# Kernel tuning notes

Hardware: AMD Instinct MI355X
Metric: run time of the kernel (lower is better)

Reference implementation:

```python
import jax, jax.numpy as jnp
import numpy as np

H = 8192  # hidden_size == input_size
NNZ = 1_000_000
B = 128
T = 64


def _spmm(rows, cols, values, x, out_dim):
    # y[r, :] += v * x[c, :] for each nnz (r, c, v); matches coalesced COO spmm
    gathered = values[:, None] * x[cols]          # [nnz, B]
    return jax.ops.segment_sum(gathered, rows, num_segments=out_dim)  # [out_dim, B]


def setup_inputs() -> dict:
    key = jax.random.key(0)
    ks = jax.random.split(key, 5)
    x = jax.random.normal(ks[0], (B, T, H), dtype=jnp.float32)
    ih_indices = jax.random.randint(ks[1], (2, NNZ), 0, H, dtype=jnp.int32)
    hh_indices = jax.random.randint(ks[2], (2, NNZ), 0, H, dtype=jnp.int32)
    # scale so tanh pre-activations stay in a reasonable range (~122 nnz/row)
    ih_values = jax.random.normal(ks[3], (NNZ,), dtype=jnp.float32) * 0.05
    hh_values = jax.random.normal(ks[4], (NNZ,), dtype=jnp.float32) * 0.05
    bias_ih = jnp.zeros((H, 1), dtype=jnp.float32)
    bias_hh = jnp.zeros((H, 1), dtype=jnp.float32)
    return {
        "x": x,
        "ih_indices": ih_indices,
        "ih_values": ih_values,
        "hh_indices": hh_indices,
        "hh_values": hh_values,
        "bias_ih": bias_ih,
        "bias_hh": bias_hh,
    }


def reference(x, ih_indices, ih_values, hh_indices, hh_values, bias_ih, bias_hh):
    # x: (batch, seq, features) -> (T, F, B) as in torch permute(1, 2, 0)
    xs = jnp.transpose(x, (1, 2, 0))  # [T, H, B]
    ih_r, ih_c = ih_indices[0], ih_indices[1]
    hh_r, hh_c = hh_indices[0], hh_indices[1]

    def step(h, x_t):
        pre = (_spmm(ih_r, ih_c, ih_values, x_t, H) + bias_ih
               + _spmm(hh_r, hh_c, hh_values, h, H) + bias_hh)
        h_new = jnp.tanh(pre)
        return h_new, h_new

    h0 = jnp.zeros((H, x.shape[0]), dtype=x.dtype)
    _, out = jax.lax.scan(step, h0, xs)  # out: [T, H, B]
    return jnp.transpose(out, (2, 0, 1))  # [B, T, H] (batch_first)
```

## Files before the change

kernel.cpp:

```cpp
#include <hip/hip_runtime.h>
#include <cstdint>
#include <cstddef>
#include <cstring>

#define H 8192
#define NNZ 1000000
#define B 128
#define T 64

typedef unsigned int u32;
typedef float f32x4 __attribute__((ext_vector_type(4)));

__device__ inline float bf_lo(u32 w) { return __uint_as_float(w << 16); }
__device__ inline float bf_hi(u32 w) { return __uint_as_float(w & 0xffff0000u); }
__device__ inline unsigned short f2bf(float f) {
    u32 v = __float_as_uint(f);
    v += 0x7fffu + ((v >> 16) & 1u);
    return (unsigned short)(v >> 16);
}
__device__ inline u32 pack_bf16(float a, float b) {
    return (u32)f2bf(a) | ((u32)f2bf(b) << 16);
}
__device__ inline float fast_tanh(float x) {
    float e = __expf(2.0f * x);
    return 1.0f - 2.0f / (e + 1.0f);
}

__global__ void hist_kernel(const int* __restrict__ rows, int nnz, int* __restrict__ count) {
    int j = blockIdx.x * blockDim.x + threadIdx.x;
    if (j < nnz) atomicAdd(&count[rows[j]], 1);
}

__global__ void scan_kernel(const int* __restrict__ cnt0, int* __restrict__ rp0, int* __restrict__ cur0,
                            const int* __restrict__ cnt1, int* __restrict__ rp1, int* __restrict__ cur1) {
    const int* cnt = (blockIdx.x == 0) ? cnt0 : cnt1;
    int* rp  = (blockIdx.x == 0) ? rp0 : rp1;
    int* cur = (blockIdx.x == 0) ? cur0 : cur1;
    __shared__ int buf[1024];
    __shared__ int carry;
    int tid = threadIdx.x;
    if (tid == 0) carry = 0;
    __syncthreads();
    for (int base = 0; base < H; base += 1024) {
        int v = cnt[base + tid];
        buf[tid] = v;
        __syncthreads();
        for (int off = 1; off < 1024; off <<= 1) {
            int t = (tid >= off) ? buf[tid - off] : 0;
            __syncthreads();
            buf[tid] += t;
            __syncthreads();
        }
        int incl = buf[tid];
        int excl = incl - v;
        int c = carry;
        rp[base + tid]  = c + excl;
        cur[base + tid] = c + excl;
        __syncthreads();
        if (tid == 1023) carry = c + incl;
        __syncthreads();
    }
    if (tid == 0) rp[H] = carry;
}

__global__ void scatter_kernel(const int* __restrict__ rows, const int* __restrict__ cols,
                               const float* __restrict__ vals, int nnz,
                               int* __restrict__ cursor, int2* __restrict__ opair) {
    int j = blockIdx.x * blockDim.x + threadIdx.x;
    if (j < nnz) {
        int r = rows[j];
        int p = atomicAdd(&cursor[r], 1);
        opair[p] = make_int2(cols[j], __float_as_int(vals[j]));
    }
}

__global__ void transpose_kernel(const float* __restrict__ src, float* __restrict__ dst,
                                 int R, int C) {
    __shared__ float tile[32][33];
    int c0 = blockIdx.x * 32, r0 = blockIdx.y * 32;
    int x = threadIdx.x, y = threadIdx.y;
    #pragma unroll
    for (int i = y; i < 32; i += 8) {
        tile[i][x] = src[(size_t)(r0 + i) * C + (c0 + x)];
    }
    __syncthreads();
    #pragma unroll
    for (int i = y; i < 32; i += 8) {
        dst[(size_t)(c0 + i) * R + (r0 + x)] = tile[x][i];
    }
}

__global__ void transpose_bf16_kernel(const float* __restrict__ src, u32* __restrict__ dst) {
    __shared__ float tile[32][33];
    int c0 = blockIdx.x * 32;
    int r0 = blockIdx.y * 32;
    int x = threadIdx.x, y = threadIdx.y;
    #pragma unroll
    for (int i = y; i < 32; i += 8) {
        tile[i][x] = src[(size_t)(r0 + i) * (T * H) + (c0 + x)];
    }
    __syncthreads();
    int tid = y * 32 + x;
    #pragma unroll
    for (int idx = tid; idx < 32 * 16; idx += 256) {
        int row = idx >> 4, w = idx & 15;
        u32 word = pack_bf16(tile[2 * w][row], tile[2 * w + 1][row]);
        dst[(size_t)(c0 + row) * 64 + (r0 >> 1) + w] = word;
    }
}

__global__ void __launch_bounds__(64) ih_pre_kernel(
    const int* __restrict__ rp, const int2* __restrict__ pair,
    const u32* __restrict__ xTb, float* __restrict__ pre,
    const float* __restrict__ bias_ih, const float* __restrict__ bias_hh) {
    int bid = blockIdx.x;
    int xcd = bid & 7;
    int i0  = bid >> 3;
    int t   = (xcd << 3) + (i0 >> 13);
    int r   = i0 & (H - 1);
    int lane = threadIdx.x;
    bool hi = lane >= 32;
    int i = lane & 31;
    const uint2* __restrict__ xt = (const uint2*)(xTb + (size_t)t * H * 64);
    f32x4 acc = {0.f, 0.f, 0.f, 0.f};
    int s = rp[r], e = rp[r + 1];
    int j = s;
    for (; j + 16 <= e; j += 16) {
        int2 q[16];
        #pragma unroll
        for (int u = 0; u < 16; ++u) q[u] = pair[j + u];
        uint2 g[8];
        #pragma unroll
        for (int u = 0; u < 8; ++u) {
            int c = hi ? q[2 * u + 1].x : q[2 * u].x;
            g[u] = xt[(size_t)c * 32 + i];
        }
        #pragma unroll
        for (int u = 0; u < 8; ++u) {
            float v = __int_as_float(hi ? q[2 * u + 1].y : q[2 * u].y);
            acc.x = fmaf(v, bf_lo(g[u].x), acc.x);
            acc.y = fmaf(v, bf_hi(g[u].x), acc.y);
            acc.z = fmaf(v, bf_lo(g[u].y), acc.z);
            acc.w = fmaf(v, bf_hi(g[u].y), acc.w);
        }
    }
    for (; j + 2 <= e; j += 2) {
        int2 q0 = pair[j], q1 = pair[j + 1];
        int c = hi ? q1.x : q0.x;
        uint2 g = xt[(size_t)c * 32 + i];
        float v = __int_as_float(hi ? q1.y : q0.y);
        acc.x = fmaf(v, bf_lo(g.x), acc.x);
        acc.y = fmaf(v, bf_hi(g.x), acc.y);
        acc.z = fmaf(v, bf_lo(g.y), acc.z);
        acc.w = fmaf(v, bf_hi(g.y), acc.w);
    }
    if (j < e) {
        int2 q0 = pair[j];
        uint2 g = xt[(size_t)q0.x * 32 + i];
        float v = hi ? 0.0f : __int_as_float(q0.y);
        acc.x = fmaf(v, bf_lo(g.x), acc.x);
        acc.y = fmaf(v, bf_hi(g.x), acc.y);
        acc.z = fmaf(v, bf_lo(g.y), acc.z);
        acc.w = fmaf(v, bf_hi(g.y), acc.w);
    }
    f32x4 tot;
    tot.x = acc.x + __shfl_xor(acc.x, 32, 64);
    tot.y = acc.y + __shfl_xor(acc.y, 32, 64);
    tot.z = acc.z + __shfl_xor(acc.z, 32, 64);
    tot.w = acc.w + __shfl_xor(acc.w, 32, 64);
    if (lane < 32) {
        float bias = bias_ih[r] + bias_hh[r];
        tot.x += bias; tot.y += bias; tot.z += bias; tot.w += bias;
        __builtin_nontemporal_store(tot, (f32x4*)(pre + ((size_t)t * H + r) * B) + i);
    }
}

__global__ void __launch_bounds__(64) step_kernel(
    const int* __restrict__ rp, const int2* __restrict__ pair,
    const u32* __restrict__ hprev, u32* __restrict__ hnew, float* __restrict__ pre_t) {
    int r = blockIdx.x;
    int lane = threadIdx.x;
    bool hi = lane >= 32;
    int i = lane & 31;
    const uint2* __restrict__ hp = (const uint2*)hprev;
    f32x4 acc = {0.f, 0.f, 0.f, 0.f};
    int s = rp[r], e = rp[r + 1];
    int j = s;
    for (; j + 16 <= e; j += 16) {
        int2 q[16];
        #pragma unroll
        for (int u = 0; u < 16; ++u) q[u] = pair[j + u];
        uint2 g[8];
        #pragma unroll
        for (int u = 0; u < 8; ++u) {
            int c = hi ? q[2 * u + 1].x : q[2 * u].x;
            g[u] = hp[(size_t)c * 32 + i];
        }
        #pragma unroll
        for (int u = 0; u < 8; ++u) {
            float v = __int_as_float(hi ? q[2 * u + 1].y : q[2 * u].y);
            acc.x = fmaf(v, bf_lo(g[u].x), acc.x);
            acc.y = fmaf(v, bf_hi(g[u].x), acc.y);
            acc.z = fmaf(v, bf_lo(g[u].y), acc.z);
            acc.w = fmaf(v, bf_hi(g[u].y), acc.w);
        }
    }
    for (; j + 2 <= e; j += 2) {
        int2 q0 = pair[j], q1 = pair[j + 1];
        int c = hi ? q1.x : q0.x;
        uint2 g = hp[(size_t)c * 32 + i];
        float v = __int_as_float(hi ? q1.y : q0.y);
        acc.x = fmaf(v, bf_lo(g.x), acc.x);
        acc.y = fmaf(v, bf_hi(g.x), acc.y);
        acc.z = fmaf(v, bf_lo(g.y), acc.z);
        acc.w = fmaf(v, bf_hi(g.y), acc.w);
    }
    if (j < e) {
        int2 q0 = pair[j];
        uint2 g = hp[(size_t)q0.x * 32 + i];
        float v = hi ? 0.0f : __int_as_float(q0.y);
        acc.x = fmaf(v, bf_lo(g.x), acc.x);
        acc.y = fmaf(v, bf_hi(g.x), acc.y);
        acc.z = fmaf(v, bf_lo(g.y), acc.z);
        acc.w = fmaf(v, bf_hi(g.y), acc.w);
    }
    f32x4 tot;
    tot.x = acc.x + __shfl_xor(acc.x, 32, 64);
    tot.y = acc.y + __shfl_xor(acc.y, 32, 64);
    tot.z = acc.z + __shfl_xor(acc.z, 32, 64);
    tot.w = acc.w + __shfl_xor(acc.w, 32, 64);
    if (lane < 32) {
        f32x4 p = __builtin_nontemporal_load((const f32x4*)(pre_t + (size_t)r * B) + i);
        float h0 = fast_tanh(tot.x + p.x);
        float h1 = fast_tanh(tot.y + p.y);
        float h2 = fast_tanh(tot.z + p.z);
        float h3 = fast_tanh(tot.w + p.w);
        f32x4 o = {h0, h1, h2, h3};
        __builtin_nontemporal_store(o, (f32x4*)(pre_t + (size_t)r * B) + i);
        uint2 hw;
        hw.x = pack_bf16(h0, h1);
        hw.y = pack_bf16(h2, h3);
        ((uint2*)hnew)[(size_t)r * 32 + i] = hw;
    }
}

extern "C" void kernel_launch(void* const* d_in, const int* in_sizes, int n_in,
                              void* d_out, int out_size, void* d_ws, size_t ws_size,
                              hipStream_t stream) {
    const float* x        = (const float*)d_in[0];
    const int*   ih_idx   = (const int*)d_in[1];
    const float* ih_val   = (const float*)d_in[2];
    const int*   hh_idx   = (const int*)d_in[3];
    const float* hh_val   = (const float*)d_in[4];
    const float* bias_ih  = (const float*)d_in[5];
    const float* bias_hh  = (const float*)d_in[6];
    const int* ih_rows = ih_idx;
    const int* ih_cols = ih_idx + NNZ;
    const int* hh_rows = hh_idx;
    const int* hh_cols = hh_idx + NNZ;

    char* ws = (char*)d_ws;
    size_t off = 0;
    auto alloc = [&](size_t bytes) -> void* {
        void* p = ws + off;
        off += (bytes + 255) & ~(size_t)255;
        return p;
    };
    u32*   xTb     = (u32*)  alloc((size_t)T * H * 64 * 4);
    float* pre     = (float*)alloc((size_t)T * H * B * 4);
    int2*  pair_ih = (int2*) alloc((size_t)NNZ * 8);
    int2*  pair_hh = (int2*) alloc((size_t)NNZ * 8);
    int*   rp_ih   = (int*)  alloc((size_t)(H + 1) * 4);
    int*   rp_hh   = (int*)  alloc((size_t)(H + 1) * 4);
    int*   cnt_ih  = (int*)  alloc((size_t)H * 4);
    int*   cnt_hh  = (int*)  alloc((size_t)H * 4);
    int*   cur_ih  = (int*)  alloc((size_t)H * 4);
    int*   cur_hh  = (int*)  alloc((size_t)H * 4);
    u32*   h0      = (u32*)  alloc((size_t)H * 64 * 4);
    u32*   h1      = (u32*)  alloc((size_t)H * 64 * 4);

    hipMemsetAsync(cnt_ih, 0, (size_t)H * 4, stream);
    hipMemsetAsync(cnt_hh, 0, (size_t)H * 4, stream);
    hipMemsetAsync(h0, 0, (size_t)H * 64 * 4, stream);

    const int tb = 256;
    const int gb = (NNZ + tb - 1) / tb;
    hist_kernel<<<gb, tb, 0, stream>>>(ih_rows, NNZ, cnt_ih);
    hist_kernel<<<gb, tb, 0, stream>>>(hh_rows, NNZ, cnt_hh);
    scan_kernel<<<2, 1024, 0, stream>>>(cnt_ih, rp_ih, cur_ih, cnt_hh, rp_hh, cur_hh);
    scatter_kernel<<<gb, tb, 0, stream>>>(ih_rows, ih_cols, ih_val, NNZ, cur_ih, pair_ih);
    scatter_kernel<<<gb, tb, 0, stream>>>(hh_rows, hh_cols, hh_val, NNZ, cur_hh, pair_hh);

    dim3 tblk(32, 8);
    dim3 tgrid1((T * H) / 32, B / 32);
    transpose_bf16_kernel<<<tgrid1, tblk, 0, stream>>>(x, xTb);

    ih_pre_kernel<<<T * H, 64, 0, stream>>>(rp_ih, pair_ih, xTb, pre, bias_ih, bias_hh);

    u32* hbuf[2] = { h0, h1 };
    for (int t = 0; t < T; ++t) {
        step_kernel<<<H, 64, 0, stream>>>(rp_hh, pair_hh,
                                          hbuf[t & 1], hbuf[(t + 1) & 1],
                                          pre + (size_t)t * H * B);
    }

    dim3 tgrid2(B / 32, (T * H) / 32);
    transpose_kernel<<<tgrid2, tblk, 0, stream>>>(pre, (float*)d_out, T * H, B);
}
```

Baseline: 2.854 ms.

## Fuse per-timestep recurrent launches into one persistent cooperative kernel with grid sync

Replaces the 64 separate step_kernel launches with a single cooperative kernel that loops over timesteps and separates them with grid.sync(). Each 256-thread block holds four wavefronts and strides over rows, so the hidden-state ping-pong happens inside the kernel. The aim is to remove per-launch overhead and the gaps between dependent kernel launches. The costs are a grid-wide barrier per step, fewer resident waves, and the requirement that all blocks are co-resident: the grid size is derived from the occupancy query times 256 CUs and capped at 2048.

```diff
diff --git a/kernel.cpp b/kernel.cpp
--- a/kernel.cpp
+++ b/kernel.cpp
@@ -1,7 +1,10 @@
 #include <hip/hip_runtime.h>
+#include <hip/hip_cooperative_groups.h>
 #include <cstdint>
 #include <cstddef>
 #include <cstring>
+
+namespace cg = cooperative_groups;
 
 #define H 8192
 #define NNZ 1000000
@@ -175,72 +178,85 @@
     }
 }
 
-__global__ void __launch_bounds__(64) step_kernel(
+__global__ void __launch_bounds__(256, 8) coop_steps_kernel(
     const int* __restrict__ rp, const int2* __restrict__ pair,
-    const u32* __restrict__ hprev, u32* __restrict__ hnew, float* __restrict__ pre_t) {
-    int r = blockIdx.x;
-    int lane = threadIdx.x;
-    bool hi = lane >= 32;
-    int i = lane & 31;
-    const uint2* __restrict__ hp = (const uint2*)hprev;
-    f32x4 acc = {0.f, 0.f, 0.f, 0.f};
-    int s = rp[r], e = rp[r + 1];
-    int j = s;
-    for (; j + 16 <= e; j += 16) {
-        int2 q[16];
-        #pragma unroll
-        for (int u = 0; u < 16; ++u) q[u] = pair[j + u];
-        uint2 g[8];
-        #pragma unroll
-        for (int u = 0; u < 8; ++u) {
-            int c = hi ? q[2 * u + 1].x : q[2 * u].x;
-            g[u] = hp[(size_t)c * 32 + i];
+    u32* __restrict__ ha, u32* __restrict__ hb, float* __restrict__ pre) {
+    cg::grid_group grid = cg::this_grid();
+    const int tid  = threadIdx.x;
+    const int wav  = tid >> 6;
+    const int lane = tid & 63;
+    const bool hi  = lane >= 32;
+    const int i    = lane & 31;
+    const int rstride = (int)(gridDim.x << 2);
+    u32* hp = ha;
+    u32* hn = hb;
+    for (int t = 0; t < T; ++t) {
+        float* __restrict__ pre_t = pre + (size_t)t * H * B;
+        const uint2* __restrict__ h2 = (const uint2*)hp;
+        for (int r0 = ((int)blockIdx.x << 2) + wav; r0 < H; r0 += rstride) {
+            const int r = __builtin_amdgcn_readfirstlane(r0);
+            f32x4 acc = {0.f, 0.f, 0.f, 0.f};
+            int s = rp[r], e = rp[r + 1];
+            int j = s;
+            for (; j + 16 <= e; j += 16) {
+                int2 q[16];
+                #pragma unroll
+                for (int u = 0; u < 16; ++u) q[u] = pair[j + u];
+                uint2 g[8];
+                #pragma unroll
+                for (int u = 0; u < 8; ++u) {
+                    int c = hi ? q[2 * u + 1].x : q[2 * u].x;
+                    g[u] = h2[(size_t)c * 32 + i];
+                }
+                #pragma unroll
+                for (int u = 0; u < 8; ++u) {
+                    float v = __int_as_float(hi ? q[2 * u + 1].y : q[2 * u].y);
+                    acc.x = fmaf(v, bf_lo(g[u].x), acc.x);
+                    acc.y = fmaf(v, bf_hi(g[u].x), acc.y);
+                    acc.z = fmaf(v, bf_lo(g[u].y), acc.z);
+                    acc.w = fmaf(v, bf_hi(g[u].y), acc.w);
+                }
+            }
+            for (; j + 2 <= e; j += 2) {
+                int2 q0 = pair[j], q1 = pair[j + 1];
+                int c = hi ? q1.x : q0.x;
+                uint2 g = h2[(size_t)c * 32 + i];
+                float v = __int_as_float(hi ? q1.y : q0.y);
+                acc.x = fmaf(v, bf_lo(g.x), acc.x);
+                acc.y = fmaf(v, bf_hi(g.x), acc.y);
+                acc.z = fmaf(v, bf_lo(g.y), acc.z);
+                acc.w = fmaf(v, bf_hi(g.y), acc.w);
+            }
+            if (j < e) {
+                int2 q0 = pair[j];
+                uint2 g = h2[(size_t)q0.x * 32 + i];
+                float v = hi ? 0.0f : __int_as_float(q0.y);
+                acc.x = fmaf(v, bf_lo(g.x), acc.x);
+                acc.y = fmaf(v, bf_hi(g.x), acc.y);
+                acc.z = fmaf(v, bf_lo(g.y), acc.z);
+                acc.w = fmaf(v, bf_hi(g.y), acc.w);
+            }
+            f32x4 tot;
+            tot.x = acc.x + __shfl_xor(acc.x, 32, 64);
+            tot.y = acc.y + __shfl_xor(acc.y, 32, 64);
+            tot.z = acc.z + __shfl_xor(acc.z, 32, 64);
+            tot.w = acc.w + __shfl_xor(acc.w, 32, 64);
+            if (lane < 32) {
+                f32x4 p = __builtin_nontemporal_load((const f32x4*)(pre_t + (size_t)r * B) + i);
+                float h0 = fast_tanh(tot.x + p.x);
+                float h1 = fast_tanh(tot.y + p.y);
+                float h2v = fast_tanh(tot.z + p.z);
+                float h3 = fast_tanh(tot.w + p.w);
+                f32x4 o = {h0, h1, h2v, h3};
+                __builtin_nontemporal_store(o, (f32x4*)(pre_t + (size_t)r * B) + i);
+                uint2 hw;
+                hw.x = pack_bf16(h0, h1);
+                hw.y = pack_bf16(h2v, h3);
+                ((uint2*)hn)[(size_t)r * 32 + i] = hw;
+            }
         }
-        #pragma unroll
-        for (int u = 0; u < 8; ++u) {
-            float v = __int_as_float(hi ? q[2 * u + 1].y : q[2 * u].y);
-            acc.x = fmaf(v, bf_lo(g[u].x), acc.x);
-            acc.y = fmaf(v, bf_hi(g[u].x), acc.y);
-            acc.z = fmaf(v, bf_lo(g[u].y), acc.z);
-            acc.w = fmaf(v, bf_hi(g[u].y), acc.w);
-        }
-    }
-    for (; j + 2 <= e; j += 2) {
-        int2 q0 = pair[j], q1 = pair[j + 1];
-        int c = hi ? q1.x : q0.x;
-        uint2 g = hp[(size_t)c * 32 + i];
-        float v = __int_as_float(hi ? q1.y : q0.y);
-        acc.x = fmaf(v, bf_lo(g.x), acc.x);
-        acc.y = fmaf(v, bf_hi(g.x), acc.y);
-        acc.z = fmaf(v, bf_lo(g.y), acc.z);
-        acc.w = fmaf(v, bf_hi(g.y), acc.w);
-    }
-    if (j < e) {
-        int2 q0 = pair[j];
-        uint2 g = hp[(size_t)q0.x * 32 + i];
-        float v = hi ? 0.0f : __int_as_float(q0.y);
-        acc.x = fmaf(v, bf_lo(g.x), acc.x);
-        acc.y = fmaf(v, bf_hi(g.x), acc.y);
-        acc.z = fmaf(v, bf_lo(g.y), acc.z);
-        acc.w = fmaf(v, bf_hi(g.y), acc.w);
-    }
-    f32x4 tot;
-    tot.x = acc.x + __shfl_xor(acc.x, 32, 64);
-    tot.y = acc.y + __shfl_xor(acc.y, 32, 64);
-    tot.z = acc.z + __shfl_xor(acc.z, 32, 64);
-    tot.w = acc.w + __shfl_xor(acc.w, 32, 64);
-    if (lane < 32) {
-        f32x4 p = __builtin_nontemporal_load((const f32x4*)(pre_t + (size_t)r * B) + i);
-        float h0 = fast_tanh(tot.x + p.x);
-        float h1 = fast_tanh(tot.y + p.y);
-        float h2 = fast_tanh(tot.z + p.z);
-        float h3 = fast_tanh(tot.w + p.w);
-        f32x4 o = {h0, h1, h2, h3};
-        __builtin_nontemporal_store(o, (f32x4*)(pre_t + (size_t)r * B) + i);
-        uint2 hw;
-        hw.x = pack_bf16(h0, h1);
-        hw.y = pack_bf16(h2, h3);
-        ((uint2*)hnew)[(size_t)r * 32 + i] = hw;
+        grid.sync();
+        u32* tmp = hp; hp = hn; hn = tmp;
     }
 }
 
@@ -297,11 +313,17 @@
 
     ih_pre_kernel<<<T * H, 64, 0, stream>>>(rp_ih, pair_ih, xTb, pre, bias_ih, bias_hh);
 
-    u32* hbuf[2] = { h0, h1 };
-    for (int t = 0; t < T; ++t) {
-        step_kernel<<<H, 64, 0, stream>>>(rp_hh, pair_hh,
-                                          hbuf[t & 1], hbuf[(t + 1) & 1],
-                                          pre + (size_t)t * H * B);
+    {
+        int maxB = 0;
+        hipOccupancyMaxActiveBlocksPerMultiprocessor(&maxB, (const void*)coop_steps_kernel, 256, 0);
+        int nblk = maxB * 256;
+        if (nblk > 2048) nblk = 2048;
+        if (nblk < 64)   nblk = 64;
+        const int* rp_a = rp_hh; const int2* pair_a = pair_hh;
+        u32* ha = h0; u32* hb = h1; float* pre_a = pre;
+        void* args[] = { (void*)&rp_a, (void*)&pair_a, (void*)&ha, (void*)&hb, (void*)&pre_a };
+        hipLaunchCooperativeKernel((const void*)coop_steps_kernel, dim3(nblk), dim3(256),
+                                   args, 0, stream);
     }
 
     dim3 tgrid2(B / 32, (T * H) / 32);
```

New measurement: 11.17 ms. 291% more time.

## Store pre-activations and outputs in bf16 and pack four rows per step block

Applied to the files above, without the earlier changes.

The input-projection pre-activations are now stored as bf16 instead of fp32, halving that buffer's traffic. The hidden states are written straight into a per-timestep bf16 output buffer instead of ping-pong buffers, so the step kernel no longer writes fp32 outputs. The final transpose reads bf16 and expands it to fp32. Step blocks now hold four waves, one row each, and the t=0 step skips the SpMM on a zero hidden state. Rounding pre-activations and final outputs to bf16 loses precision.

```diff
diff --git a/kernel.cpp b/kernel.cpp
--- a/kernel.cpp
+++ b/kernel.cpp
@@ -10,6 +10,7 @@
 
 typedef unsigned int u32;
 typedef float f32x4 __attribute__((ext_vector_type(4)));
+typedef u32 u32x2 __attribute__((ext_vector_type(2)));
 
 __device__ inline float bf_lo(u32 w) { return __uint_as_float(w << 16); }
 __device__ inline float bf_hi(u32 w) { return __uint_as_float(w & 0xffff0000u); }
@@ -74,22 +75,6 @@
     }
 }
 
-__global__ void transpose_kernel(const float* __restrict__ src, float* __restrict__ dst,
-                                 int R, int C) {
-    __shared__ float tile[32][33];
-    int c0 = blockIdx.x * 32, r0 = blockIdx.y * 32;
-    int x = threadIdx.x, y = threadIdx.y;
-    #pragma unroll
-    for (int i = y; i < 32; i += 8) {
-        tile[i][x] = src[(size_t)(r0 + i) * C + (c0 + x)];
-    }
-    __syncthreads();
-    #pragma unroll
-    for (int i = y; i < 32; i += 8) {
-        dst[(size_t)(c0 + i) * R + (r0 + x)] = tile[x][i];
-    }
-}
-
 __global__ void transpose_bf16_kernel(const float* __restrict__ src, u32* __restrict__ dst) {
     __shared__ float tile[32][33];
     int c0 = blockIdx.x * 32;
@@ -109,9 +94,28 @@
     }
 }
 
+__global__ void transpose_out_kernel(const u32* __restrict__ src, float* __restrict__ dst) {
+    __shared__ u32 tile[32][33];
+    int c0 = blockIdx.x * 32;
+    int w0 = blockIdx.y * 32;
+    int x = threadIdx.x, y = threadIdx.y;
+    #pragma unroll
+    for (int i = y; i < 32; i += 8) {
+        tile[i][x] = src[(size_t)(c0 + i) * 64 + (w0 + x)];
+    }
+    __syncthreads();
+    #pragma unroll
+    for (int i = y; i < 64; i += 8) {
+        int w = i >> 1;
+        u32 word = tile[x][w];
+        float val = (i & 1) ? bf_hi(word) : bf_lo(word);
+        dst[(size_t)(2 * w0 + i) * (size_t)(T * H) + (c0 + x)] = val;
+    }
+}
+
 __global__ void __launch_bounds__(64) ih_pre_kernel(
     const int* __restrict__ rp, const int2* __restrict__ pair,
-    const u32* __restrict__ xTb, float* __restrict__ pre,
+    const u32* __restrict__ xTb, u32* __restrict__ pre,
     const float* __restrict__ bias_ih, const float* __restrict__ bias_hh) {
     int bid = blockIdx.x;
     int xcd = bid & 7;
@@ -170,77 +174,81 @@
     tot.w = acc.w + __shfl_xor(acc.w, 32, 64);
     if (lane < 32) {
         float bias = bias_ih[r] + bias_hh[r];
-        tot.x += bias; tot.y += bias; tot.z += bias; tot.w += bias;
-        __builtin_nontemporal_store(tot, (f32x4*)(pre + ((size_t)t * H + r) * B) + i);
-    }
-}
-
-__global__ void __launch_bounds__(64) step_kernel(
+        u32x2 pw;
+        pw.x = pack_bf16(tot.x + bias, tot.y + bias);
+        pw.y = pack_bf16(tot.z + bias, tot.w + bias);
+        __builtin_nontemporal_store(pw, (u32x2*)(pre + ((size_t)t * H + r) * 64) + i);
+    }
+}
+
+__global__ void __launch_bounds__(256) step_kernel(
     const int* __restrict__ rp, const int2* __restrict__ pair,
-    const u32* __restrict__ hprev, u32* __restrict__ hnew, float* __restrict__ pre_t) {
-    int r = blockIdx.x;
-    int lane = threadIdx.x;
-    bool hi = lane >= 32;
-    int i = lane & 31;
-    const uint2* __restrict__ hp = (const uint2*)hprev;
+    const u32* __restrict__ hprev, u32* __restrict__ hout,
+    const u32* __restrict__ pre_t) {
+    const int tid  = threadIdx.x;
+    const int wav  = tid >> 6;
+    const int lane = tid & 63;
+    const bool hi  = lane >= 32;
+    const int i    = lane & 31;
+    const int r = __builtin_amdgcn_readfirstlane(((int)blockIdx.x << 2) + wav);
+    u32x2 pw = __builtin_nontemporal_load((const u32x2*)pre_t + (size_t)r * 32 + i);
     f32x4 acc = {0.f, 0.f, 0.f, 0.f};
-    int s = rp[r], e = rp[r + 1];
-    int j = s;
-    for (; j + 16 <= e; j += 16) {
-        int2 q[16];
-        #pragma unroll
-        for (int u = 0; u < 16; ++u) q[u] = pair[j + u];
-        uint2 g[8];
-        #pragma unroll
-        for (int u = 0; u < 8; ++u) {
-            int c = hi ? q[2 * u + 1].x : q[2 * u].x;
-            g[u] = hp[(size_t)c * 32 + i];
-        }
-        #pragma unroll
-        for (int u = 0; u < 8; ++u) {
-            float v = __int_as_float(hi ? q[2 * u + 1].y : q[2 * u].y);
-            acc.x = fmaf(v, bf_lo(g[u].x), acc.x);
-            acc.y = fmaf(v, bf_hi(g[u].x), acc.y);
-            acc.z = fmaf(v, bf_lo(g[u].y), acc.z);
-            acc.w = fmaf(v, bf_hi(g[u].y), acc.w);
-        }
-    }
-    for (; j + 2 <= e; j += 2) {
-        int2 q0 = pair[j], q1 = pair[j + 1];
-        int c = hi ? q1.x : q0.x;
-        uint2 g = hp[(size_t)c * 32 + i];
-        float v = __int_as_float(hi ? q1.y : q0.y);
-        acc.x = fmaf(v, bf_lo(g.x), acc.x);
-        acc.y = fmaf(v, bf_hi(g.x), acc.y);
-        acc.z = fmaf(v, bf_lo(g.y), acc.z);
-        acc.w = fmaf(v, bf_hi(g.y), acc.w);
-    }
-    if (j < e) {
-        int2 q0 = pair[j];
-        uint2 g = hp[(size_t)q0.x * 32 + i];
-        float v = hi ? 0.0f : __int_as_float(q0.y);
-        acc.x = fmaf(v, bf_lo(g.x), acc.x);
-        acc.y = fmaf(v, bf_hi(g.x), acc.y);
-        acc.z = fmaf(v, bf_lo(g.y), acc.z);
-        acc.w = fmaf(v, bf_hi(g.y), acc.w);
-    }
-    f32x4 tot;
-    tot.x = acc.x + __shfl_xor(acc.x, 32, 64);
-    tot.y = acc.y + __shfl_xor(acc.y, 32, 64);
-    tot.z = acc.z + __shfl_xor(acc.z, 32, 64);
-    tot.w = acc.w + __shfl_xor(acc.w, 32, 64);
+    if (hprev) {
+        const uint2* __restrict__ h2 = (const uint2*)hprev;
+        int s = rp[r], e = rp[r + 1];
+        int j = s;
+        for (; j + 16 <= e; j += 16) {
+            int2 q[16];
+            #pragma unroll
+            for (int u = 0; u < 16; ++u) q[u] = pair[j + u];
+            uint2 g[8];
+            #pragma unroll
+            for (int u = 0; u < 8; ++u) {
+                int c = hi ? q[2 * u + 1].x : q[2 * u].x;
+                g[u] = h2[(size_t)c * 32 + i];
+            }
+            #pragma unroll
+            for (int u = 0; u < 8; ++u) {
+                float v = __int_as_float(hi ? q[2 * u + 1].y : q[2 * u].y);
+                acc.x = fmaf(v, bf_lo(g[u].x), acc.x);
+                acc.y = fmaf(v, bf_hi(g[u].x), acc.y);
+                acc.z = fmaf(v, bf_lo(g[u].y), acc.z);
+                acc.w = fmaf(v, bf_hi(g[u].y), acc.w);
+            }
+        }
+        for (; j + 2 <= e; j += 2) {
+            int2 q0 = pair[j], q1 = pair[j + 1];
+            int c = hi ? q1.x : q0.x;
+            uint2 g = h2[(size_t)c * 32 + i];
+            float v = __int_as_float(hi ? q1.y : q0.y);
+            acc.x = fmaf(v, bf_lo(g.x), acc.x);
+            acc.y = fmaf(v, bf_hi(g.x), acc.y);
+            acc.z = fmaf(v, bf_lo(g.y), acc.z);
+            acc.w = fmaf(v, bf_hi(g.y), acc.w);
+        }
+        if (j < e) {
+            int2 q0 = pair[j];
+            uint2 g = h2[(size_t)q0.x * 32 + i];
+            float v = hi ? 0.0f : __int_as_float(q0.y);
+            acc.x = fmaf(v, bf_lo(g.x), acc.x);
+            acc.y = fmaf(v, bf_hi(g.x), acc.y);
+            acc.z = fmaf(v, bf_lo(g.y), acc.z);
+            acc.w = fmaf(v, bf_hi(g.y), acc.w);
+        }
+        acc.x += __shfl_xor(acc.x, 32, 64);
+        acc.y += __shfl_xor(acc.y, 32, 64);
+        acc.z += __shfl_xor(acc.z, 32, 64);
+        acc.w += __shfl_xor(acc.w, 32, 64);
+    }
     if (lane < 32) {
-        f32x4 p = __builtin_nontemporal_load((const f32x4*)(pre_t + (size_t)r * B) + i);
-        float h0 = fast_tanh(tot.x + p.x);
-        float h1 = fast_tanh(tot.y + p.y);
-        float h2 = fast_tanh(tot.z + p.z);
-        float h3 = fast_tanh(tot.w + p.w);
-        f32x4 o = {h0, h1, h2, h3};
-        __builtin_nontemporal_store(o, (f32x4*)(pre_t + (size_t)r * B) + i);
+        float h0 = fast_tanh(acc.x + bf_lo(pw.x));
+        float h1 = fast_tanh(acc.y + bf_hi(pw.x));
+        float h2v = fast_tanh(acc.z + bf_lo(pw.y));
+        float h3 = fast_tanh(acc.w + bf_hi(pw.y));
         uint2 hw;
         hw.x = pack_bf16(h0, h1);
-        hw.y = pack_bf16(h2, h3);
-        ((uint2*)hnew)[(size_t)r * 32 + i] = hw;
+        hw.y = pack_bf16(h2v, h3);
+        ((uint2*)hout)[(size_t)r * 32 + i] = hw;
     }
 }
 
@@ -267,7 +275,8 @@
         return p;
     };
     u32*   xTb     = (u32*)  alloc((size_t)T * H * 64 * 4);
-    float* pre     = (float*)alloc((size_t)T * H * B * 4);
+    u32*   pre     = (u32*)  alloc((size_t)T * H * 64 * 4);
+    u32*   outb    = (u32*)  alloc((size_t)T * H * 64 * 4);
     int2*  pair_ih = (int2*) alloc((size_t)NNZ * 8);
     int2*  pair_hh = (int2*) alloc((size_t)NNZ * 8);
     int*   rp_ih   = (int*)  alloc((size_t)(H + 1) * 4);
@@ -276,12 +285,9 @@
     int*   cnt_hh  = (int*)  alloc((size_t)H * 4);
     int*   cur_ih  = (int*)  alloc((size_t)H * 4);
     int*   cur_hh  = (int*)  alloc((size_t)H * 4);
-    u32*   h0      = (u32*)  alloc((size_t)H * 64 * 4);
-    u32*   h1      = (u32*)  alloc((size_t)H * 64 * 4);
 
     hipMemsetAsync(cnt_ih, 0, (size_t)H * 4, stream);
     hipMemsetAsync(cnt_hh, 0, (size_t)H * 4, stream);
-    hipMemsetAsync(h0, 0, (size_t)H * 64 * 4, stream);
 
     const int tb = 256;
     const int gb = (NNZ + tb - 1) / tb;
@@ -297,13 +303,15 @@
 
     ih_pre_kernel<<<T * H, 64, 0, stream>>>(rp_ih, pair_ih, xTb, pre, bias_ih, bias_hh);
 
-    u32* hbuf[2] = { h0, h1 };
-    for (int t = 0; t < T; ++t) {
-        step_kernel<<<H, 64, 0, stream>>>(rp_hh, pair_hh,
-                                          hbuf[t & 1], hbuf[(t + 1) & 1],
-                                          pre + (size_t)t * H * B);
-    }
-
-    dim3 tgrid2(B / 32, (T * H) / 32);
-    transpose_kernel<<<tgrid2, tblk, 0, stream>>>(pre, (float*)d_out, T * H, B);
-}
+    step_kernel<<<H / 4, 256, 0, stream>>>(rp_hh, pair_hh, (const u32*)nullptr,
+                                           outb, pre);
+    for (int t = 1; t < T; ++t) {
+        step_kernel<<<H / 4, 256, 0, stream>>>(rp_hh, pair_hh,
+                                               outb + (size_t)(t - 1) * H * 64,
+                                               outb + (size_t)t * H * 64,
+                                               pre + (size_t)t * H * 64);
+    }
+
+    dim3 tgrid2((T * H) / 32, 2);
+    transpose_out_kernel<<<tgrid2, tblk, 0, stream>>>(outb, (float*)d_out);
+}
```

Result: faster. 2.622 ms (-8.1%).
